# Kernel tuning notes

Hardware: AMD Instinct MI355X
Metric: run time of the kernel (lower is better)

The kernel has to match this reference:

```python
import jax, jax.numpy as jnp
import numpy as np

B = 512        # batch of 9x9 crops
N = 5184
M = 81         # 9*9 low-res pixels
ITERS = 100    # FISTA iterations (hardcoded in original)
MU = 1.0       # self.mu constant


def setup_inputs() -> dict:
    key = jax.random.key(0)
    k1, k2 = jax.random.split(key)
    x = jax.random.normal(k1, (B, 9, 9), dtype=jnp.float32)
    # PSF measurement matrix [N, M]; random stand-in for create_psf_matrix(9, 8),
    # scaled down so the fixed 1/mu step size keeps the iteration stable.
    mat = jax.random.normal(k2, (N, M), dtype=jnp.float32) * 0.02
    lam = jnp.array([0.12], dtype=jnp.float32)  # self.lam = ones * 0.12
    return {"x": x, "mat": mat, "lam": lam}


def _softthresh(w, thr):
    # Equivalent to: where(w > thr, w - thr, 0) + where(w < -thr, w + thr, 0)
    return jnp.sign(w) * jnp.maximum(jnp.abs(w) - thr, 0.0)


def reference(x, mat, lam):
    xf = x.reshape(x.shape[0], -1)          # [B, M] flattened inputs
    thr = lam / MU                          # lam / mu, broadcast scalar

    def step(carry, _):
        y, t = carry                        # y: [B, N], t: scalar
        # re = mat @ (x - mat^T @ y), batched: matvec(mat^T, y) == y @ mat
        re = (xf - y @ mat) @ mat.T         # [B, N]
        w = y + re / MU
        y_new = _softthresh(w, thr)
        t_n = (1.0 + jnp.sqrt(1.0 + t * t)) / 2.0
        y_out = y_new + (t - 1.0) / t_n * (y_new - y)   # FISTA momentum
        return (y_out, t_n), None

    y0 = jnp.zeros((xf.shape[0], mat.shape[0]), dtype=xf.dtype)
    t0 = jnp.asarray(1.0, dtype=xf.dtype)
    (y, _), _ = jax.lax.scan(step, (y0, t0), None, length=ITERS)
    return y  # [B, N] sparse high-res reconstruction
```

## Files before the change

kernel.cpp:

```cpp
#include <hip/hip_runtime.h>
#include <math.h>

#define NN 5184
#define MM 81
#define BTOT 512
#define NITER 100
#define NSL 64
#define BSL 4
#define NR 81
#define BR 128
#define MP 84
#define KP 21
#define THREADS 1024
#define GRID (NSL*BSL)
#define PSTRIDE (BTOT*MM)
#define SMEM_FLOATS (NR*MP + BR*NR + BR*MP)
#define SMEM_BYTES (SMEM_FLOATS*4)

__global__ void init_sync(unsigned* cnt) { *cnt = 0u; }

__device__ __forceinline__ void grid_barrier(unsigned* cnt, unsigned target) {
    __syncthreads();
    if (threadIdx.x == 0) {
        __hip_atomic_fetch_add(cnt, 1u, __ATOMIC_ACQ_REL, __HIP_MEMORY_SCOPE_AGENT);
        while (__hip_atomic_load(cnt, __ATOMIC_ACQUIRE, __HIP_MEMORY_SCOPE_AGENT) < target)
            __builtin_amdgcn_s_sleep(8);
    }
    __syncthreads();
}

__global__ __launch_bounds__(THREADS, 4) void fista(
        const float* __restrict__ x, const float* __restrict__ mat,
        const float* __restrict__ lam, float* __restrict__ out,
        float* __restrict__ zbuf, unsigned* __restrict__ cnt) {
    extern __shared__ float smem[];
    float*  matLf = smem;
    float*  yL    = smem + NR*MP;
    float*  zLf   = smem + NR*MP + BR*NR;
    float4* matL4 = (float4*)matLf;
    float4* zL4   = (float4*)zLf;

    const int tid = threadIdx.x;
    const int bid = blockIdx.x;
    const int nsl = bid >> 2;
    const int bsl = bid & 3;
    const int n0  = nsl * NR;
    const int b0  = bsl * BR;
    float* partials = out;

    for (int i = tid; i < NR*MP; i += THREADS) {
        int r = i / MP, m = i - r*MP;
        matLf[i] = (m < MM) ? mat[(size_t)(n0 + r)*MM + m] : 0.f;
    }
    for (int i = tid; i < BR*NR; i += THREADS) yL[i] = 0.f;
    for (int i = tid; i < BR*MP; i += THREADS) {
        int b = i / MP, m = i - b*MP;
        zLf[i] = (m < MM) ? x[(size_t)(b0 + b)*MM + m] : 0.f;
    }
    __syncthreads();

    const float thr  = lam[0];
    const int wv = tid >> 6, lane = tid & 63;
    const int bb = wv << 3;
    const int m4 = lane % KP;
    const int ns3 = lane / KP;
    float t = 1.f;
    unsigned bar = 0;

    for (int it = 0; it < NITER; ++it) {
        float tn = (1.f + sqrtf(1.f + t*t)) * 0.5f;
        float coef = (t - 1.f) / tn;
        t = tn;

        for (int p = 0; p < 2; ++p) {
            int n = (p << 6) + lane;
            if (n < NR) {
                float re[8];
#pragma unroll
                for (int b = 0; b < 8; ++b) re[b] = 0.f;
                for (int k = 0; k < KP; ++k) {
                    float4 mv = matL4[n*KP + k];
#pragma unroll
                    for (int b = 0; b < 8; ++b) {
                        float4 zv = zL4[(bb + b)*KP + k];
                        re[b] += zv.x*mv.x + zv.y*mv.y + zv.z*mv.z + zv.w*mv.w;
                    }
                }
#pragma unroll
                for (int b = 0; b < 8; ++b) {
                    float* yp = &yL[(bb + b)*NR + n];
                    float yo = *yp;
                    float w  = yo + re[b];
                    float yn = fmaxf(w - thr, 0.f) + fminf(w + thr, 0.f);
                    *yp = yn + coef*(yn - yo);
                }
            }
        }
        if (it == NITER - 1) break;
        __syncthreads();

        {
            float4 acc[8];
#pragma unroll
            for (int b = 0; b < 8; ++b) acc[b] = float4{0.f,0.f,0.f,0.f};
            if (ns3 < 3) {
                const int nb = ns3 * 27;
                for (int s = 0; s < 27; ++s) {
                    int n = nb + s;
                    float4 mv = matL4[n*KP + m4];
#pragma unroll
                    for (int b = 0; b < 8; ++b) {
                        float yv = yL[(bb + b)*NR + n];
                        acc[b].x += yv*mv.x; acc[b].y += yv*mv.y;
                        acc[b].z += yv*mv.z; acc[b].w += yv*mv.w;
                    }
                }
            }
            for (int g = 0; g < 3; ++g) {
                if (ns3 == g) {
#pragma unroll
                    for (int b = 0; b < 8; ++b) {
                        int ui = (bb + b)*KP + m4;
                        if (g == 0) zL4[ui] = acc[b];
                        else {
                            float4 u = zL4[ui];
                            u.x += acc[b].x; u.y += acc[b].y;
                            u.z += acc[b].z; u.w += acc[b].w;
                            zL4[ui] = u;
                        }
                    }
                }
            }
        }
        __syncthreads();

        {
            size_t pbase = ((size_t)nsl*BTOT + b0) * MM;
            for (int f = tid; f < BR*MM; f += THREADS) {
                int b = f / MM, m = f - b*MM;
                partials[pbase + f] = zLf[b*MP + m];
            }
        }
        grid_barrier(cnt, ++bar * (unsigned)GRID);

        {
            float* redzf = zLf;
            if (tid < 648) {
                int e = tid >> 2, q = tid & 3;
                int blo = (e >= 81) ? 1 : 0;
                int m = e - (blo ? 81 : 0);
                int bg = b0 + 2*nsl + blo;
                const float* pp = partials + (size_t)bg*MM + m;
                float s = 0.f;
                int s0 = q << 4;
#pragma unroll 4
                for (int s2 = 0; s2 < 16; ++s2)
                    s += pp[(size_t)(s0 + s2) * PSTRIDE];
                redzf[tid] = s;
            }
            __syncthreads();
            if (tid < 162) {
                int blo = (tid >= 81) ? 1 : 0;
                int m = tid - (blo ? 81 : 0);
                int bg = b0 + 2*nsl + blo;
                float tot = redzf[tid*4] + redzf[tid*4+1] + redzf[tid*4+2] + redzf[tid*4+3];
                zbuf[(size_t)bg*MM + m] = x[(size_t)bg*MM + m] - tot;
            }
        }
        grid_barrier(cnt, ++bar * (unsigned)GRID);

        {
            size_t zbase = (size_t)b0 * MM;
            for (int f = tid; f < BR*MM; f += THREADS) {
                int b = f / MM, m = f - b*MM;
                zLf[b*MP + m] = zbuf[zbase + f];
            }
        }
        __syncthreads();
    }

    __syncthreads();
    for (int i = tid; i < BR*NR; i += THREADS) {
        int b = i / NR, n = i - b*NR;
        out[(size_t)(b0 + b)*NN + n0 + n] = yL[i];
    }
}

extern "C" void kernel_launch(void* const* d_in, const int* in_sizes, int n_in,
                              void* d_out, int out_size, void* d_ws, size_t ws_size,
                              hipStream_t stream) {
    const float* x   = (const float*)d_in[0];
    const float* mat = (const float*)d_in[1];
    const float* lam = (const float*)d_in[2];
    float* out = (float*)d_out;

    unsigned* cnt = (unsigned*)d_ws;
    float* zbuf = (float*)((char*)d_ws + 1024);

    hipFuncSetAttribute((const void*)fista,
                        hipFuncAttributeMaxDynamicSharedMemorySize, SMEM_BYTES);
    init_sync<<<1, 1, 0, stream>>>(cnt);
    fista<<<GRID, THREADS, SMEM_BYTES, stream>>>(x, mat, lam, out, zbuf, cnt);
}
```

Measured before the change: 7.305 ms.

## Restructure FISTA into per-batch-group barriers with register-resident y and atomic LDS reduction

Regroups the grid into 8 independent batch groups of 32 blocks, each syncing on its own counter instead of a full-grid barrier. Each lane keeps one batch row of z and its y slice in registers, reads mat rows directly from global memory via scalar loads, and accumulates mat^T y partials into LDS with atomics. The x-minus-reduction step now writes straight into a padded z buffer that a prefill kernel seeds with x. This removes one reload phase and shrinks barrier scope, at the cost of heavy register pressure (over 160 floats per lane), many LDS atomics, and global mat reads every iteration.

Result: slower. 28.69 ms (+292.7%).

```diff
diff --git a/kernel.cpp b/kernel.cpp
--- a/kernel.cpp
+++ b/kernel.cpp
@@ -5,26 +5,37 @@
 #define MM 81
 #define BTOT 512
 #define NITER 100
-#define NSL 64
-#define BSL 4
-#define NR 81
-#define BR 128
-#define MP 84
-#define KP 21
+#define NSL 32
+#define GRP 8
+#define NR 162
+#define BR 64
 #define THREADS 1024
-#define GRID (NSL*BSL)
-#define PSTRIDE (BTOT*MM)
-#define SMEM_FLOATS (NR*MP + BR*NR + BR*MP)
-#define SMEM_BYTES (SMEM_FLOATS*4)
+#define GRID (NSL*GRP)
+#define RMAX 11
+#define YT_STRIDE 65
+#define UL_STRIDE 85
+#define ZB_STRIDE 96
+#define SMEM_BYTES 84000
 
-__global__ void init_sync(unsigned* cnt) { *cnt = 0u; }
+
+__global__ void prefill(const float* __restrict__ x, float* __restrict__ zbuf,
+                        unsigned* __restrict__ cnt) {
+    int i = blockIdx.x * 256 + threadIdx.x;
+    if (i < GRP * BR * ZB_STRIDE) {
+        int g = i / (BR * ZB_STRIDE);
+        int r = i - g * (BR * ZB_STRIDE);
+        int b = r / ZB_STRIDE, m = r - b * ZB_STRIDE;
+        zbuf[i] = (m < MM) ? x[(size_t)(g * BR + b) * MM + m] : 0.f;
+    }
+    if (i < 1024) cnt[i] = 0u;
+}
 
 __device__ __forceinline__ void grid_barrier(unsigned* cnt, unsigned target) {
     __syncthreads();
     if (threadIdx.x == 0) {
         __hip_atomic_fetch_add(cnt, 1u, __ATOMIC_ACQ_REL, __HIP_MEMORY_SCOPE_AGENT);
         while (__hip_atomic_load(cnt, __ATOMIC_ACQUIRE, __HIP_MEMORY_SCOPE_AGENT) < target)
-            __builtin_amdgcn_s_sleep(8);
+            __builtin_amdgcn_s_sleep(2);
     }
     __syncthreads();
 }
@@ -32,157 +43,139 @@
 __global__ __launch_bounds__(THREADS, 4) void fista(
         const float* __restrict__ x, const float* __restrict__ mat,
         const float* __restrict__ lam, float* __restrict__ out,
-        float* __restrict__ zbuf, unsigned* __restrict__ cnt) {
-    extern __shared__ float smem[];
-    float*  matLf = smem;
-    float*  yL    = smem + NR*MP;
-    float*  zLf   = smem + NR*MP + BR*NR;
-    float4* matL4 = (float4*)matLf;
-    float4* zL4   = (float4*)zLf;
+        float* __restrict__ zbuf, unsigned* __restrict__ cntbase) {
+    extern __shared__ float sm[];
+    float* yT  = sm;
+    float* uL  = sm + NR * YT_STRIDE;
+    float* red = uL + BR * UL_STRIDE;
 
-    const int tid = threadIdx.x;
-    const int bid = blockIdx.x;
-    const int nsl = bid >> 2;
-    const int bsl = bid & 3;
-    const int n0  = nsl * NR;
-    const int b0  = bsl * BR;
-    float* partials = out;
+    const int tid  = threadIdx.x;
+    const int wv   = tid >> 6, lane = tid & 63;
+    const int g    = blockIdx.x & 7;
+    const int slot = blockIdx.x >> 3;
+    const int b0   = g * BR;
+    const int n0   = slot * NR;
+    const float thr = lam[0];
+    unsigned* cnt  = cntbase + g * 64;
+    unsigned* gcnt = cntbase + 512;
+    float* zb = zbuf + (size_t)g * BR * ZB_STRIDE;
+    float* pbuf = out;
 
-    for (int i = tid; i < NR*MP; i += THREADS) {
-        int r = i / MP, m = i - r*MP;
-        matLf[i] = (m < MM) ? mat[(size_t)(n0 + r)*MM + m] : 0.f;
-    }
-    for (int i = tid; i < BR*NR; i += THREADS) yL[i] = 0.f;
-    for (int i = tid; i < BR*MP; i += THREADS) {
-        int b = i / MP, m = i - b*MP;
-        zLf[i] = (m < MM) ? x[(size_t)(b0 + b)*MM + m] : 0.f;
-    }
+    for (int i = tid; i < BR * UL_STRIDE; i += THREADS) uL[i] = 0.f;
     __syncthreads();
 
-    const float thr  = lam[0];
-    const int wv = tid >> 6, lane = tid & 63;
-    const int bb = wv << 3;
-    const int m4 = lane % KP;
-    const int ns3 = lane / KP;
+    const int rbeg = wv * 10 + (wv < 2 ? wv : 2);
+    const int rcnt = (wv < 2) ? 11 : 10;
+
+    float ya[RMAX];
+#pragma unroll
+    for (int r = 0; r < RMAX; ++r) ya[r] = 0.f;
+
     float t = 1.f;
     unsigned bar = 0;
 
     for (int it = 0; it < NITER; ++it) {
-        float tn = (1.f + sqrtf(1.f + t*t)) * 0.5f;
+        float tn = (1.f + sqrtf(1.f + t * t)) * 0.5f;
         float coef = (t - 1.f) / tn;
         t = tn;
+        const bool dob = (it != NITER - 1);
 
-        for (int p = 0; p < 2; ++p) {
-            int n = (p << 6) + lane;
-            if (n < NR) {
-                float re[8];
+        float za[84];
+        {
+            const float4* zp = (const float4*)(zb + (size_t)lane * ZB_STRIDE);
 #pragma unroll
-                for (int b = 0; b < 8; ++b) re[b] = 0.f;
-                for (int k = 0; k < KP; ++k) {
-                    float4 mv = matL4[n*KP + k];
+            for (int i = 0; i < 21; ++i) {
+                float4 v = zp[i];
+                za[4*i] = v.x; za[4*i+1] = v.y; za[4*i+2] = v.z; za[4*i+3] = v.w;
+            }
+        }
+
+        float ua[MM];
+        if (dob) {
 #pragma unroll
-                    for (int b = 0; b < 8; ++b) {
-                        float4 zv = zL4[(bb + b)*KP + k];
-                        re[b] += zv.x*mv.x + zv.y*mv.y + zv.z*mv.z + zv.w*mv.w;
-                    }
+            for (int m = 0; m < MM; ++m) ua[m] = 0.f;
+        }
+
+#pragma unroll
+        for (int r = 0; r < RMAX; ++r) {
+            if (r < rcnt) {
+                const float* mrow = mat +
+                    (size_t)__builtin_amdgcn_readfirstlane(n0 + rbeg + r) * MM;
+                float re0 = 0.f, re1 = 0.f, re2 = 0.f, re3 = 0.f;
+#pragma unroll
+                for (int m = 0; m < 80; m += 4) {
+                    re0 = fmaf(mrow[m],     za[m],     re0);
+                    re1 = fmaf(mrow[m + 1], za[m + 1], re1);
+                    re2 = fmaf(mrow[m + 2], za[m + 2], re2);
+                    re3 = fmaf(mrow[m + 3], za[m + 3], re3);
                 }
+                re0 = fmaf(mrow[80], za[80], re0);
+                float re = (re0 + re1) + (re2 + re3);
+                float yo = ya[r];
+                float w  = yo + re;
+                float yn = fmaxf(w - thr, 0.f) + fminf(w + thr, 0.f);
+                float yv = yn + coef * (yn - yo);
+                ya[r] = yv;
+                if (dob) {
 #pragma unroll
-                for (int b = 0; b < 8; ++b) {
-                    float* yp = &yL[(bb + b)*NR + n];
-                    float yo = *yp;
-                    float w  = yo + re[b];
-                    float yn = fmaxf(w - thr, 0.f) + fminf(w + thr, 0.f);
-                    *yp = yn + coef*(yn - yo);
+                    for (int m = 0; m < MM; ++m)
+                        ua[m] = fmaf(mrow[m], yv, ua[m]);
                 }
             }
         }
-        if (it == NITER - 1) break;
+        if (!dob) break;
+
+#pragma unroll
+        for (int m = 0; m < MM; ++m)
+            __hip_atomic_fetch_add(&uL[lane * UL_STRIDE + m], ua[m],
+                                   __ATOMIC_RELAXED, __HIP_MEMORY_SCOPE_WORKGROUP);
         __syncthreads();
 
         {
-            float4 acc[8];
-#pragma unroll
-            for (int b = 0; b < 8; ++b) acc[b] = float4{0.f,0.f,0.f,0.f};
-            if (ns3 < 3) {
-                const int nb = ns3 * 27;
-                for (int s = 0; s < 27; ++s) {
-                    int n = nb + s;
-                    float4 mv = matL4[n*KP + m4];
-#pragma unroll
-                    for (int b = 0; b < 8; ++b) {
-                        float yv = yL[(bb + b)*NR + n];
-                        acc[b].x += yv*mv.x; acc[b].y += yv*mv.y;
-                        acc[b].z += yv*mv.z; acc[b].w += yv*mv.w;
-                    }
-                }
-            }
-            for (int g = 0; g < 3; ++g) {
-                if (ns3 == g) {
-#pragma unroll
-                    for (int b = 0; b < 8; ++b) {
-                        int ui = (bb + b)*KP + m4;
-                        if (g == 0) zL4[ui] = acc[b];
-                        else {
-                            float4 u = zL4[ui];
-                            u.x += acc[b].x; u.y += acc[b].y;
-                            u.z += acc[b].z; u.w += acc[b].w;
-                            zL4[ui] = u;
-                        }
-                    }
-                }
+            size_t base = (((size_t)g * NSL + slot) * BR) * MM;
+            for (int i = tid; i < BR * MM; i += THREADS) {
+                int b = i / MM, m = i - b * MM;
+                pbuf[base + i] = uL[b * UL_STRIDE + m];
             }
         }
         __syncthreads();
+        for (int i = tid; i < BR * UL_STRIDE; i += THREADS) uL[i] = 0.f;
 
-        {
-            size_t pbase = ((size_t)nsl*BTOT + b0) * MM;
-            for (int f = tid; f < BR*MM; f += THREADS) {
-                int b = f / MM, m = f - b*MM;
-                partials[pbase + f] = zLf[b*MP + m];
-            }
-        }
-        grid_barrier(cnt, ++bar * (unsigned)GRID);
+        grid_barrier(cnt, ++bar * 32u);
 
-        {
-            float* redzf = zLf;
-            if (tid < 648) {
-                int e = tid >> 2, q = tid & 3;
-                int blo = (e >= 81) ? 1 : 0;
-                int m = e - (blo ? 81 : 0);
-                int bg = b0 + 2*nsl + blo;
-                const float* pp = partials + (size_t)bg*MM + m;
-                float s = 0.f;
-                int s0 = q << 4;
-#pragma unroll 4
-                for (int s2 = 0; s2 < 16; ++s2)
-                    s += pp[(size_t)(s0 + s2) * PSTRIDE];
-                redzf[tid] = s;
-            }
-            __syncthreads();
-            if (tid < 162) {
-                int blo = (tid >= 81) ? 1 : 0;
-                int m = tid - (blo ? 81 : 0);
-                int bg = b0 + 2*nsl + blo;
-                float tot = redzf[tid*4] + redzf[tid*4+1] + redzf[tid*4+2] + redzf[tid*4+3];
-                zbuf[(size_t)bg*MM + m] = x[(size_t)bg*MM + m] - tot;
-            }
-        }
-        grid_barrier(cnt, ++bar * (unsigned)GRID);
-
-        {
-            size_t zbase = (size_t)b0 * MM;
-            for (int f = tid; f < BR*MM; f += THREADS) {
-                int b = f / MM, m = f - b*MM;
-                zLf[b*MP + m] = zbuf[zbase + f];
-            }
+        if (tid < 648) {
+            int sq = tid & 3, e = tid >> 2;
+            int b2 = (e >= MM) ? 1 : 0;
+            int m  = e - b2 * MM;
+            int bg = 2 * slot + b2;
+            const float* pp = pbuf + (((size_t)g * NSL) * BR + bg) * MM + m;
+            float ssum = 0.f;
+#pragma unroll
+            for (int s2 = 0; s2 < 8; ++s2)
+                ssum += pp[(size_t)(sq * 8 + s2) * BR * MM];
+            red[tid] = ssum;
         }
         __syncthreads();
+        if (tid < 162) {
+            int b2 = (tid >= MM) ? 1 : 0;
+            int m  = tid - b2 * MM;
+            int bg = 2 * slot + b2;
+            float tot = red[tid*4] + red[tid*4+1] + red[tid*4+2] + red[tid*4+3];
+            zb[(size_t)bg * ZB_STRIDE + m] = x[(size_t)(b0 + bg) * MM + m] - tot;
+        }
+
+        grid_barrier(cnt, ++bar * 32u);
     }
 
+    grid_barrier(gcnt, (unsigned)GRID);
+
+#pragma unroll
+    for (int r = 0; r < RMAX; ++r)
+        if (r < rcnt) yT[(rbeg + r) * YT_STRIDE + lane] = ya[r];
     __syncthreads();
-    for (int i = tid; i < BR*NR; i += THREADS) {
-        int b = i / NR, n = i - b*NR;
-        out[(size_t)(b0 + b)*NN + n0 + n] = yL[i];
+    for (int i = tid; i < BR * NR; i += THREADS) {
+        int b = i / NR, n = i - b * NR;
+        out[(size_t)(b0 + b) * NN + n0 + n] = yT[n * YT_STRIDE + b];
     }
 }
 
@@ -195,10 +188,10 @@
     float* out = (float*)d_out;
 
     unsigned* cnt = (unsigned*)d_ws;
-    float* zbuf = (float*)((char*)d_ws + 1024);
+    float* zbuf   = (float*)((char*)d_ws + 4096);
 
     hipFuncSetAttribute((const void*)fista,
                         hipFuncAttributeMaxDynamicSharedMemorySize, SMEM_BYTES);
-    init_sync<<<1, 1, 0, stream>>>(cnt);
+    prefill<<<(GRP * BR * ZB_STRIDE + 255) / 256, 256, 0, stream>>>(x, zbuf, cnt);
     fista<<<GRID, THREADS, SMEM_BYTES, stream>>>(x, mat, lam, out, zbuf, cnt);
 }
```
